# Performance work log

Hardware: AMD Instinct MI355X
Metric: run time of the kernel (lower is better)

Reference implementation:

```python
import jax, jax.numpy as jnp
import numpy as np


def setup_inputs() -> dict:
    key0 = jax.random.key(0)
    kq, kk, kv = jax.random.split(key0, 3)
    B, S, D = 16, 2048, 64  # batch*heads, seq_len, head_dim
    return {
        "query": jax.random.normal(kq, (B, S, D), dtype=jnp.float32),
        "key": jax.random.normal(kk, (B, S, D), dtype=jnp.float32),
        "value": jax.random.normal(kv, (B, S, D), dtype=jnp.float32),
    }


def reference(query, key, value):
    # context = K @ V^T : [B, S, S]  (the seq x seq intermediate the kernel should avoid)
    context = jnp.einsum("bkd,bvd->bkv", key, value)
    # attention = context^T @ Q : [B, S, D]
    attention = jnp.einsum("bkv,bkd->bvd", context, query)
    return attention
```

## Files before the change

### kernel.cpp

```cpp
#include <hip/hip_runtime.h>


typedef float vf4 __attribute__((ext_vector_type(4)));

#define BATCH 16
#define SEQ   2048
#define DIM   64
#define SCHUNK 128
#define NCHUNK (SEQ / SCHUNK)
#define ROWS2  128
#define TPADR  132

__global__ __launch_bounds__(256, 2) void ktq_part_kernel(
        const float* __restrict__ K, const float* __restrict__ Q,
        float* __restrict__ P) {
    __shared__ float Ks[SCHUNK * DIM];
    __shared__ float Qs[SCHUNK * DIM];
    const int b     = blockIdx.y;
    const int chunk = blockIdx.x;
    const int t     = threadIdx.x;

    const float* Kb = K + ((size_t)b * SEQ + (size_t)chunk * SCHUNK) * DIM;
    const float* Qb = Q + ((size_t)b * SEQ + (size_t)chunk * SCHUNK) * DIM;

#pragma unroll
    for (int i = 0; i < 8; ++i) {
        int idx = i * 256 + t;
        ((vf4*)Ks)[idx] = ((const vf4*)Kb)[idx];
        ((vf4*)Qs)[idx] = ((const vf4*)Qb)[idx];
    }
    __syncthreads();

    const int tx = t & 15;
    const int ty = t >> 4;
    float acc[4][4] = {};

    for (int s = 0; s < SCHUNK; ++s) {
        vf4 ak = *(const vf4*)&Ks[s * DIM + ty * 4];
        vf4 bq = *(const vf4*)&Qs[s * DIM + tx * 4];
#pragma unroll
        for (int i = 0; i < 4; ++i)
#pragma unroll
            for (int j = 0; j < 4; ++j) acc[i][j] += ak[i] * bq[j];
    }

    float* Pb = P + ((size_t)b * NCHUNK + chunk) * DIM * DIM;
#pragma unroll
    for (int i = 0; i < 4; ++i) {
        vf4 r = {acc[i][0], acc[i][1], acc[i][2], acc[i][3]};
        *(vf4*)&Pb[(ty * 4 + i) * DIM + tx * 4] = r;
    }
}

__global__ __launch_bounds__(512) void vm_red_kernel(
        const float* __restrict__ V, const float* __restrict__ P,
        float* __restrict__ O) {
    __shared__ float Ml[DIM * DIM];
    __shared__ float VsT[DIM * TPADR];
    const int b  = blockIdx.y;
    const int rb = blockIdx.x;
    const int t  = threadIdx.x;

    const float* Pb = P + (size_t)b * NCHUNK * DIM * DIM;
#pragma unroll
    for (int i = 0; i < 2; ++i) {
        int idx = i * 512 + t;
        vf4 sum = ((const vf4*)Pb)[idx];
#pragma unroll
        for (int c = 1; c < NCHUNK; ++c)
            sum += ((const vf4*)(Pb + (size_t)c * DIM * DIM))[idx];
        ((vf4*)Ml)[idx] = sum;
    }

    const float* Vb = V + ((size_t)b * SEQ + (size_t)rb * ROWS2) * DIM;
#pragma unroll
    for (int i = 0; i < 4; ++i) {
        int idx = i * 512 + t;
        int row = idx >> 4;
        int col = (idx & 15) * 4;
        vf4 v = ((const vf4*)Vb)[idx];
        VsT[(col + 0) * TPADR + row] = v[0];
        VsT[(col + 1) * TPADR + row] = v[1];
        VsT[(col + 2) * TPADR + row] = v[2];
        VsT[(col + 3) * TPADR + row] = v[3];
    }
    __syncthreads();

    const int tx = t & 15;
    const int ty = t >> 4;
    float acc[4][4] = {};

    for (int dp = 0; dp < DIM; ++dp) {
        vf4 mv = *(const vf4*)&Ml[dp * DIM + tx * 4];
        vf4 av = *(const vf4*)&VsT[dp * TPADR + ty * 4];
#pragma unroll
        for (int i = 0; i < 4; ++i)
#pragma unroll
            for (int j = 0; j < 4; ++j) acc[i][j] += av[i] * mv[j];
    }

    float* Ob = O + ((size_t)b * SEQ + (size_t)rb * ROWS2) * DIM;
#pragma unroll
    for (int i = 0; i < 4; ++i) {
        vf4 o = {acc[i][0], acc[i][1], acc[i][2], acc[i][3]};
        __builtin_nontemporal_store(o, (vf4*)&Ob[(ty * 4 + i) * DIM + tx * 4]);
    }
}

extern "C" void kernel_launch(void* const* d_in, const int* in_sizes, int n_in,
                              void* d_out, int out_size, void* d_ws, size_t ws_size,
                              hipStream_t stream) {
    const float* Q = (const float*)d_in[0];
    const float* K = (const float*)d_in[1];
    const float* V = (const float*)d_in[2];
    float* O = (float*)d_out;
    float* P = (float*)d_ws;

    dim3 gridA(NCHUNK, BATCH);
    ktq_part_kernel<<<gridA, 256, 0, stream>>>(K, Q, P);

    dim3 gridB(SEQ / ROWS2, BATCH);
    vm_red_kernel<<<gridB, 512, 0, stream>>>(V, P, O);
}
```

Baseline: 86.37 us.

## Split reduction dimension across thread groups with shared-memory partial-sum reduction

Both kernels now launch 1024 threads per block, splitting the inner reduction loop (sequence chunk in the first, head dimension in the second) across 4 or 2 thread groups. The partial 4x4 tiles are combined through shared memory before the final global store. The intent is to raise the number of waves per CU, since the grid has only as many blocks as CUs, and so hide memory and LDS latency better. In exchange it adds extra barriers, shared-memory traffic for the reduction, and idle threads during the final combine.

```diff
diff --git a/kernel.cpp b/kernel.cpp
--- a/kernel.cpp
+++ b/kernel.cpp
@@ -10,12 +10,14 @@
 #define NCHUNK (SEQ / SCHUNK)
 #define ROWS2  128
 #define TPADR  132
+#define RPAD   68
 
-__global__ __launch_bounds__(256, 2) void ktq_part_kernel(
+__global__ __launch_bounds__(1024, 1) void ktq_part_kernel(
         const float* __restrict__ K, const float* __restrict__ Q,
         float* __restrict__ P) {
-    __shared__ float Ks[SCHUNK * DIM];
-    __shared__ float Qs[SCHUNK * DIM];
+    __shared__ __attribute__((aligned(16))) float Smem[2 * SCHUNK * DIM];
+    float* Ks = Smem;
+    float* Qs = Smem + SCHUNK * DIM;
     const int b     = blockIdx.y;
     const int chunk = blockIdx.x;
     const int t     = threadIdx.x;
@@ -24,58 +26,76 @@
     const float* Qb = Q + ((size_t)b * SEQ + (size_t)chunk * SCHUNK) * DIM;
 
 #pragma unroll
-    for (int i = 0; i < 8; ++i) {
-        int idx = i * 256 + t;
+    for (int i = 0; i < 2; ++i) {
+        int idx = i * 1024 + t;
         ((vf4*)Ks)[idx] = ((const vf4*)Kb)[idx];
         ((vf4*)Qs)[idx] = ((const vf4*)Qb)[idx];
     }
     __syncthreads();
 
-    const int tx = t & 15;
-    const int ty = t >> 4;
+    const int g   = t >> 8;
+    const int sub = t & 255;
+    const int tx  = sub & 15;
+    const int ty  = sub >> 4;
     float acc[4][4] = {};
 
-    for (int s = 0; s < SCHUNK; ++s) {
-        vf4 ak = *(const vf4*)&Ks[s * DIM + ty * 4];
-        vf4 bq = *(const vf4*)&Qs[s * DIM + tx * 4];
+    const float* KsG = Ks + (g * 32) * DIM;
+    const float* QsG = Qs + (g * 32) * DIM;
+#pragma unroll 4
+    for (int s = 0; s < 32; ++s) {
+        vf4 ak = *(const vf4*)&KsG[s * DIM + ty * 4];
+        vf4 bq = *(const vf4*)&QsG[s * DIM + tx * 4];
 #pragma unroll
         for (int i = 0; i < 4; ++i)
 #pragma unroll
             for (int j = 0; j < 4; ++j) acc[i][j] += ak[i] * bq[j];
     }
 
-    float* Pb = P + ((size_t)b * NCHUNK + chunk) * DIM * DIM;
+    __syncthreads();
+    float* Rs = Smem;
+    if (g != 0) {
 #pragma unroll
-    for (int i = 0; i < 4; ++i) {
-        vf4 r = {acc[i][0], acc[i][1], acc[i][2], acc[i][3]};
-        *(vf4*)&Pb[(ty * 4 + i) * DIM + tx * 4] = r;
+        for (int i = 0; i < 4; ++i) {
+            vf4 r = {acc[i][0], acc[i][1], acc[i][2], acc[i][3]};
+            *(vf4*)&Rs[((g - 1) * 64 + ty * 4 + i) * RPAD + tx * 4] = r;
+        }
+    }
+    __syncthreads();
+    if (g == 0) {
+        float* Pb = P + ((size_t)b * NCHUNK + chunk) * DIM * DIM;
+#pragma unroll
+        for (int i = 0; i < 4; ++i) {
+            vf4 sum = {acc[i][0], acc[i][1], acc[i][2], acc[i][3]};
+#pragma unroll
+            for (int g2 = 0; g2 < 3; ++g2)
+                sum += *(const vf4*)&Rs[(g2 * 64 + ty * 4 + i) * RPAD + tx * 4];
+            *(vf4*)&Pb[(ty * 4 + i) * DIM + tx * 4] = sum;
+        }
     }
 }
 
-__global__ __launch_bounds__(512) void vm_red_kernel(
+__global__ __launch_bounds__(1024, 1) void vm_red_kernel(
         const float* __restrict__ V, const float* __restrict__ P,
         float* __restrict__ O) {
-    __shared__ float Ml[DIM * DIM];
-    __shared__ float VsT[DIM * TPADR];
+    __shared__ __attribute__((aligned(16))) float Ml[DIM * DIM];
+    __shared__ __attribute__((aligned(16))) float VsT[DIM * TPADR];
     const int b  = blockIdx.y;
     const int rb = blockIdx.x;
     const int t  = threadIdx.x;
 
     const float* Pb = P + (size_t)b * NCHUNK * DIM * DIM;
-#pragma unroll
-    for (int i = 0; i < 2; ++i) {
-        int idx = i * 512 + t;
-        vf4 sum = ((const vf4*)Pb)[idx];
+    {
+        vf4 sum = ((const vf4*)Pb)[t];
 #pragma unroll
         for (int c = 1; c < NCHUNK; ++c)
-            sum += ((const vf4*)(Pb + (size_t)c * DIM * DIM))[idx];
-        ((vf4*)Ml)[idx] = sum;
+            sum += ((const vf4*)(Pb + (size_t)c * DIM * DIM))[t];
+        ((vf4*)Ml)[t] = sum;
     }
 
     const float* Vb = V + ((size_t)b * SEQ + (size_t)rb * ROWS2) * DIM;
 #pragma unroll
-    for (int i = 0; i < 4; ++i) {
-        int idx = i * 512 + t;
+    for (int i = 0; i < 2; ++i) {
+        int idx = i * 1024 + t;
         int row = idx >> 4;
         int col = (idx & 15) * 4;
         vf4 v = ((const vf4*)Vb)[idx];
@@ -86,11 +106,15 @@
     }
     __syncthreads();
 
-    const int tx = t & 15;
-    const int ty = t >> 4;
+    const int g   = t >> 9;
+    const int sub = t & 511;
+    const int tx  = sub & 15;
+    const int ty  = sub >> 4;
     float acc[4][4] = {};
 
-    for (int dp = 0; dp < DIM; ++dp) {
+#pragma unroll 4
+    for (int d0 = 0; d0 < 32; ++d0) {
+        int dp = g * 32 + d0;
         vf4 mv = *(const vf4*)&Ml[dp * DIM + tx * 4];
         vf4 av = *(const vf4*)&VsT[dp * TPADR + ty * 4];
 #pragma unroll
@@ -99,11 +123,25 @@
             for (int j = 0; j < 4; ++j) acc[i][j] += av[i] * mv[j];
     }
 
-    float* Ob = O + ((size_t)b * SEQ + (size_t)rb * ROWS2) * DIM;
+    __syncthreads();
+    float* Rs = VsT;
+    if (g == 1) {
 #pragma unroll
-    for (int i = 0; i < 4; ++i) {
-        vf4 o = {acc[i][0], acc[i][1], acc[i][2], acc[i][3]};
-        __builtin_nontemporal_store(o, (vf4*)&Ob[(ty * 4 + i) * DIM + tx * 4]);
+        for (int i = 0; i < 4; ++i) {
+            vf4 r = {acc[i][0], acc[i][1], acc[i][2], acc[i][3]};
+            *(vf4*)&Rs[(ty * 4 + i) * DIM + tx * 4] = r;
+        }
+    }
+    __syncthreads();
+    if (g == 0) {
+        float* Ob = O + ((size_t)b * SEQ + (size_t)rb * ROWS2) * DIM;
+#pragma unroll
+        for (int i = 0; i < 4; ++i) {
+            vf4 r = *(const vf4*)&Rs[(ty * 4 + i) * DIM + tx * 4];
+            vf4 o = {acc[i][0] + r[0], acc[i][1] + r[1],
+                     acc[i][2] + r[2], acc[i][3] + r[3]};
+            __builtin_nontemporal_store(o, (vf4*)&Ob[(ty * 4 + i) * DIM + tx * 4]);
+        }
     }
 }
 
@@ -117,8 +155,8 @@
     float* P = (float*)d_ws;
 
     dim3 gridA(NCHUNK, BATCH);
-    ktq_part_kernel<<<gridA, 256, 0, stream>>>(K, Q, P);
+    ktq_part_kernel<<<gridA, 1024, 0, stream>>>(K, Q, P);
 
     dim3 gridB(SEQ / ROWS2, BATCH);
-    vm_red_kernel<<<gridB, 512, 0, stream>>>(V, P, O);
+    vm_red_kernel<<<gridB, 1024, 0, stream>>>(V, P, O);
 }
```

Result: no change. 86.62 us (+0.3%).

## Read K, Q and V tiles directly from global memory instead of LDS staging

Applied to the files above, without the earlier changes.

Both kernels drop their shared-memory staging of input tiles. The first kernel now loads K and Q vectors straight from global memory inside the reduction loop, and the second reads V rows directly from global memory with 4-wide dot steps against the LDS-resident reduced matrix, removing the transposed VsT buffer. This removes LDS writes, a barrier and bank-conflict cost, and raises occupancy through lower LDS use. In exchange it relies on L1/L2 caching for the repeated reads across threads and makes loads less coalesced, since V reads are strided by rows per thread.

```diff
diff --git a/kernel.cpp b/kernel.cpp
--- a/kernel.cpp
+++ b/kernel.cpp
@@ -9,35 +9,24 @@
 #define SCHUNK 128
 #define NCHUNK (SEQ / SCHUNK)
 #define ROWS2  128
-#define TPADR  132
 
-__global__ __launch_bounds__(256, 2) void ktq_part_kernel(
+__global__ __launch_bounds__(256) void ktq_part_kernel(
         const float* __restrict__ K, const float* __restrict__ Q,
         float* __restrict__ P) {
-    __shared__ float Ks[SCHUNK * DIM];
-    __shared__ float Qs[SCHUNK * DIM];
     const int b     = blockIdx.y;
     const int chunk = blockIdx.x;
     const int t     = threadIdx.x;
+    const int tx    = t & 15;
+    const int ty    = t >> 4;
 
-    const float* Kb = K + ((size_t)b * SEQ + (size_t)chunk * SCHUNK) * DIM;
-    const float* Qb = Q + ((size_t)b * SEQ + (size_t)chunk * SCHUNK) * DIM;
+    const float* Kb = K + ((size_t)b * SEQ + (size_t)chunk * SCHUNK) * DIM + ty * 4;
+    const float* Qb = Q + ((size_t)b * SEQ + (size_t)chunk * SCHUNK) * DIM + tx * 4;
 
-#pragma unroll
-    for (int i = 0; i < 8; ++i) {
-        int idx = i * 256 + t;
-        ((vf4*)Ks)[idx] = ((const vf4*)Kb)[idx];
-        ((vf4*)Qs)[idx] = ((const vf4*)Qb)[idx];
-    }
-    __syncthreads();
-
-    const int tx = t & 15;
-    const int ty = t >> 4;
     float acc[4][4] = {};
-
+#pragma unroll 8
     for (int s = 0; s < SCHUNK; ++s) {
-        vf4 ak = *(const vf4*)&Ks[s * DIM + ty * 4];
-        vf4 bq = *(const vf4*)&Qs[s * DIM + tx * 4];
+        vf4 ak = *(const vf4*)&Kb[s * DIM];
+        vf4 bq = *(const vf4*)&Qb[s * DIM];
 #pragma unroll
         for (int i = 0; i < 4; ++i)
 #pragma unroll
@@ -55,8 +44,7 @@
 __global__ __launch_bounds__(512) void vm_red_kernel(
         const float* __restrict__ V, const float* __restrict__ P,
         float* __restrict__ O) {
-    __shared__ float Ml[DIM * DIM];
-    __shared__ float VsT[DIM * TPADR];
+    __shared__ __attribute__((aligned(16))) float Ml[DIM * DIM];
     const int b  = blockIdx.y;
     const int rb = blockIdx.x;
     const int t  = threadIdx.x;
@@ -71,32 +59,28 @@
             sum += ((const vf4*)(Pb + (size_t)c * DIM * DIM))[idx];
         ((vf4*)Ml)[idx] = sum;
     }
-
-    const float* Vb = V + ((size_t)b * SEQ + (size_t)rb * ROWS2) * DIM;
-#pragma unroll
-    for (int i = 0; i < 4; ++i) {
-        int idx = i * 512 + t;
-        int row = idx >> 4;
-        int col = (idx & 15) * 4;
-        vf4 v = ((const vf4*)Vb)[idx];
-        VsT[(col + 0) * TPADR + row] = v[0];
-        VsT[(col + 1) * TPADR + row] = v[1];
-        VsT[(col + 2) * TPADR + row] = v[2];
-        VsT[(col + 3) * TPADR + row] = v[3];
-    }
     __syncthreads();
 
     const int tx = t & 15;
     const int ty = t >> 4;
+    const float* Vb = V + ((size_t)b * SEQ + (size_t)rb * ROWS2 + ty * 4) * DIM;
+
     float acc[4][4] = {};
-
-    for (int dp = 0; dp < DIM; ++dp) {
-        vf4 mv = *(const vf4*)&Ml[dp * DIM + tx * 4];
-        vf4 av = *(const vf4*)&VsT[dp * TPADR + ty * 4];
+#pragma unroll 4
+    for (int dpc = 0; dpc < DIM / 4; ++dpc) {
+        vf4 m0 = *(const vf4*)&Ml[(dpc * 4 + 0) * DIM + tx * 4];
+        vf4 m1 = *(const vf4*)&Ml[(dpc * 4 + 1) * DIM + tx * 4];
+        vf4 m2 = *(const vf4*)&Ml[(dpc * 4 + 2) * DIM + tx * 4];
+        vf4 m3 = *(const vf4*)&Ml[(dpc * 4 + 3) * DIM + tx * 4];
 #pragma unroll
-        for (int i = 0; i < 4; ++i)
+        for (int i = 0; i < 4; ++i) {
+            vf4 v = *(const vf4*)&Vb[i * DIM + dpc * 4];
 #pragma unroll
-            for (int j = 0; j < 4; ++j) acc[i][j] += av[i] * mv[j];
+            for (int j = 0; j < 4; ++j) {
+                acc[i][j] += v[0] * m0[j] + v[1] * m1[j]
+                           + v[2] * m2[j] + v[3] * m3[j];
+            }
+        }
     }
 
     float* Ob = O + ((size_t)b * SEQ + (size_t)rb * ROWS2) * DIM;
```

Measured after the change: 96.54 us. 1.12x slower.
